# Kernel tuning notes

Hardware: AMD Instinct MI355X
Metric: run time of the kernel (lower is better)

## Reference

```python
import jax, jax.numpy as jnp
import numpy as np

LAMBDA_ENTROPY = 0.1
LAMBDA_REPULSION = 0.5
LAMBDA_INTER = 0.3
TEMPERATURE = 1.0
EPS = 1e-8


def setup_inputs() -> dict:
    key = jax.random.key(0)
    k1, k2 = jax.random.split(key)
    membership = jax.random.uniform(k1, (16384, 64, 32), dtype=jnp.float32)   # (N,F,K) soft bin assignments
    teacher_preds = jax.random.uniform(k2, (16384, 128), dtype=jnp.float32)   # (N,C)
    return {"membership": membership, "teacher_preds": teacher_preds}


def reference(membership, teacher_preds):
    N, F, K = membership.shape
    # --- weighted centroids per (feature, bin) ---
    bin_mass = membership.sum(axis=0) + EPS                       # (F,K)
    sum_weighted_y = jnp.einsum('nfk,nc->fkc', membership, teacher_preds)  # avoids (N,F,K,C)
    centroids = sum_weighted_y / bin_mass[..., None]              # (F,K,C)
    # --- weighted intra-bin variance: ||y_n - c_fk||^2 expanded, no (N,F,K,C) tensor ---
    y_sq = jnp.sum(teacher_preds * teacher_preds, axis=-1)        # (N,)
    c_sq = jnp.sum(centroids * centroids, axis=-1)                # (F,K)
    cross = jnp.einsum('nc,fkc->nfk', teacher_preds, centroids)   # (N,F,K)
    dist_sq = y_sq[:, None, None] + c_sq[None, :, :] - 2.0 * cross
    weighted_variance = jnp.sum(membership * dist_sq, axis=0) / bin_mass  # (F,K)
    loss_dispersion = weighted_variance.sum()
    # --- bin-occupancy entropy ---
    p_bins = bin_mass / N                                         # (F,K)
    loss_entropy = jnp.sum(p_bins * jnp.log(p_bins + EPS))
    # --- neighbor repulsion between adjacent bin centroids ---
    neighbor_dist = jnp.sum((centroids[:, :-1, :] - centroids[:, 1:, :]) ** 2, axis=-1)  # (F,K-1)
    loss_repulsion = jnp.sum(jnp.exp(-neighbor_dist / TEMPERATURE))
    # --- all-pairs inter-bin dispersion, batched over F (replaces python loop) ---
    dots = jnp.einsum('fkc,fjc->fkj', centroids, centroids)       # (F,K,K)
    pairwise = c_sq[:, :, None] + c_sq[:, None, :] - 2.0 * dots
    triu = jnp.triu(jnp.ones((K, K), dtype=centroids.dtype), k=1)  # strictly upper
    loss_inter = jnp.sum(jnp.exp(-pairwise / TEMPERATURE) * triu) / F
    total = (loss_dispersion
             + LAMBDA_ENTROPY * loss_entropy
             + LAMBDA_REPULSION * loss_repulsion
             + LAMBDA_INTER * loss_inter)
    return total, loss_dispersion, loss_entropy, loss_repulsion, loss_inter
```

## Files before the change

### kernel.cpp

```cpp
#include <hip/hip_runtime.h>
#include <math.h>

#define N_PTS   16384
#define F_DIM   64
#define K_BINS  32
#define C_DIM   128
#define FK      2048
#define NB32    (N_PTS / 32)
#define CW      132
#define EPS_F   1e-8f
#define NCHUNK  16
#define CN      1024

typedef _Float16 f16x8 __attribute__((ext_vector_type(8)));
typedef float    f32x4 __attribute__((ext_vector_type(4)));

__global__ __launch_bounds__(256) void build_ybf_k(const float* __restrict__ Y,
                                                   _Float16* __restrict__ Ybf,
                                                   float* __restrict__ accs) {
    __shared__ __align__(16) float Yl[64][132];
    __shared__ float ysql[64];
    const int t  = threadIdx.x;
    if (blockIdx.x == 0 && t < 8) accs[t] = 0.0f;
    const int n0 = blockIdx.x * 64;
    const int nl = t >> 5;
    const int c4 = t & 31;
#pragma unroll
    for (int p = 0; p < 8; ++p) {
        const int n = p * 8 + nl;
        const float4 v = reinterpret_cast<const float4*>(Y + (size_t)(n0 + n) * C_DIM)[c4];
        reinterpret_cast<float4*>(Yl[n])[c4] = v;
        float sq = v.x * v.x + v.y * v.y + v.z * v.z + v.w * v.w;
#pragma unroll
        for (int m = 16; m >= 1; m >>= 1) sq += __shfl_xor(sq, m, 64);
        if (c4 == 0) ysql[n] = sq;
    }
    __syncthreads();
    for (int p = 0; p < 5; ++p) {
        const int s = t + p * 256;
        if (s < 1152) {
            const int nb2  = s / 576;
            const int r    = s % 576;
            const int ct   = r >> 6;
            const int l    = r & 63;
            const int quad = l >> 4, cl = l & 15;
            const int nloc = nb2 * 32 + quad * 8;
            f16x8 v;
            if (ct < 8) {
                const int c = ct * 16 + cl;
#pragma unroll
                for (int j = 0; j < 8; ++j) v[j] = (_Float16)Yl[nloc + j][c];
            } else if (cl == 0) {
#pragma unroll
                for (int j = 0; j < 8; ++j) v[j] = (_Float16)ysql[nloc + j];
            } else if (cl == 1) {
#pragma unroll
                for (int j = 0; j < 8; ++j) v[j] = (_Float16)1.0f;
            } else {
#pragma unroll
                for (int j = 0; j < 8; ++j) v[j] = (_Float16)0.0f;
            }
            const int nb = blockIdx.x * 2 + nb2;
            *reinterpret_cast<f16x8*>(Ybf + ((size_t)(ct * NB32 + nb) * 64 + l) * 8) = v;
        }
    }
}

__global__ __launch_bounds__(256) void gemm_k(const float* __restrict__ M,
                                              const _Float16* __restrict__ Ybf,
                                              float* __restrict__ wpart) {
    __shared__ __align__(16) _Float16 Bb[2][2][9][512];
    const int t    = threadIdx.x;
    const int fk0  = blockIdx.x * 32;
    const int ch   = blockIdx.y;
    const int w    = t >> 6;
    const int g    = w >> 1;
    const int wl   = w & 1;
    const int l    = t & 63;
    const int quad = l >> 4;
    const int cl   = l & 15;
    const int fkA  = fk0 + wl * 16 + cl;
    const float* mp = M + fkA;
    const int n0   = ch * CN + g * 512;
    const int nb0  = n0 >> 5;

    f32x4 acc[9] = {};
    float ar[3][8];

#define WAITVM(n) asm volatile("s_waitcnt vmcnt(" #n ")" ::: "memory")
#define STAGE(s, par)                                                          \
    {                                                                          \
        const int nb_ = nb0 + (s);                                             \
        _Pragma("unroll")                                                      \
        for (int ct = wl; ct < 9; ct += 2) {                                   \
            const _Float16* g_ = Ybf + ((size_t)(ct * NB32 + nb_) * 64 + l) * 8; \
            __builtin_amdgcn_global_load_lds(                                  \
                (const __attribute__((address_space(1))) unsigned*)g_,         \
                (__attribute__((address_space(3))) unsigned*)&Bb[g][par][ct][0], \
                16, 0, 0);                                                     \
        }                                                                      \
    }
#define LOADA(s)                                                               \
    {                                                                          \
        const size_t nbase_ = (size_t)(n0 + (s) * 32 + quad * 8);              \
        _Pragma("unroll")                                                      \
        for (int j = 0; j < 8; ++j) ar[(s) % 3][j] = mp[(nbase_ + j) * FK];    \
    }
#define SBAR0() __builtin_amdgcn_sched_barrier(0)

    STAGE(0, 0); SBAR0(); LOADA(0); SBAR0();
    STAGE(1, 1); SBAR0(); LOADA(1); SBAR0(); LOADA(2); SBAR0();

#pragma unroll
    for (int s = 0; s < 16; ++s) {
        if (s < 14)       WAITVM(20);
        else if (s == 14) WAITVM(12);
        else              WAITVM(0);
        __builtin_amdgcn_s_barrier();
        SBAR0();
        f16x8 bf[9];
#pragma unroll
        for (int ct = 0; ct < 9; ++ct)
            bf[ct] = *reinterpret_cast<const f16x8*>(&Bb[g][s & 1][ct][l * 8]);
        f16x8 af;
#pragma unroll
        for (int j = 0; j < 8; ++j) af[j] = (_Float16)ar[s % 3][j];
        asm volatile("s_waitcnt lgkmcnt(0)" ::: "memory");
        SBAR0();
        __builtin_amdgcn_s_barrier();
        SBAR0();
        if (s + 2 < 16) STAGE(s + 2, s & 1);
        SBAR0();
        if (s + 3 < 16) LOADA(s + 3);
        SBAR0();
        __builtin_amdgcn_s_setprio(1);
#pragma unroll
        for (int ct = 0; ct < 9; ++ct)
            acc[ct] = __builtin_amdgcn_mfma_f32_16x16x32_f16(af, bf[ct], acc[ct], 0, 0, 0);
        __builtin_amdgcn_s_setprio(0);
    }
#undef WAITVM
#undef STAGE
#undef LOADA
#undef SBAR0

    __syncthreads();
    float* scr = reinterpret_cast<float*>(&Bb[0][0][0][0]);
    if (g == 1) {
#pragma unroll
        for (int ct = 0; ct < 9; ++ct)
#pragma unroll
            for (int r = 0; r < 4; ++r)
                scr[(wl * 16 + quad * 4 + r) * 144 + ct * 16 + cl] = acc[ct][r];
    }
    __syncthreads();
    if (g == 0) {
        float* wp = wpart + (size_t)ch * FK * CW;
#pragma unroll
        for (int ct = 0; ct < 9; ++ct) {
            const int c = ct * 16 + cl;
            if (c < CW) {
#pragma unroll
                for (int r = 0; r < 4; ++r) {
                    const int row = wl * 16 + quad * 4 + r;
                    const int fk  = fk0 + row;
                    wp[(size_t)fk * CW + c] = acc[ct][r] + scr[row * 144 + c];
                }
            }
        }
    }
}

__global__ __launch_bounds__(128) void reduce_w_k(const float* __restrict__ wpart,
                                                  float* __restrict__ W, int nchunk) {
    const int idx = blockIdx.x * 128 + threadIdx.x;
    const float4* src = reinterpret_cast<const float4*>(wpart);
    const size_t cs = (size_t)FK * CW / 4;
    float4 s0 = make_float4(0.f, 0.f, 0.f, 0.f), s1 = s0, s2 = s0, s3 = s0;
    int ch = 0;
    for (; ch + 3 < nchunk; ch += 4) {
        const float4 a = src[idx + (size_t)(ch + 0) * cs];
        const float4 b = src[idx + (size_t)(ch + 1) * cs];
        const float4 c = src[idx + (size_t)(ch + 2) * cs];
        const float4 d = src[idx + (size_t)(ch + 3) * cs];
        s0.x += a.x; s0.y += a.y; s0.z += a.z; s0.w += a.w;
        s1.x += b.x; s1.y += b.y; s1.z += b.z; s1.w += b.w;
        s2.x += c.x; s2.y += c.y; s2.z += c.z; s2.w += c.w;
        s3.x += d.x; s3.y += d.y; s3.z += d.z; s3.w += d.w;
    }
    for (; ch < nchunk; ++ch) {
        const float4 a = src[idx + (size_t)ch * cs];
        s0.x += a.x; s0.y += a.y; s0.z += a.z; s0.w += a.w;
    }
    float4 r;
    r.x = (s0.x + s1.x) + (s2.x + s3.x);
    r.y = (s0.y + s1.y) + (s2.y + s3.y);
    r.z = (s0.z + s1.z) + (s2.z + s3.z);
    r.w = (s0.w + s1.w) + (s2.w + s3.w);
    reinterpret_cast<float4*>(W)[idx] = r;
}

__global__ __launch_bounds__(256) void epilogue_k(const float* __restrict__ W,
                                                  float* __restrict__ accs,
                                                  float* __restrict__ out) {
    __shared__ __align__(16) float Wl[32][CW];
    __shared__ float Bv[32], Binv[32], S1v[32], csq[32];
    __shared__ float scr[32][8];
    __shared__ float4 red4[256];
    const int t = threadIdx.x;
    const int f = blockIdx.x;

    for (int e = t; e < 32 * 33; e += 256) {
        const int k = e / 33, c4 = e % 33;
        reinterpret_cast<float4*>(Wl[k])[c4] =
            reinterpret_cast<const float4*>(W + (size_t)(f * 32 + k) * CW)[c4];
    }
    __syncthreads();
    if (t < 32) {
        const float B = Wl[t][129] + EPS_F;
        Bv[t] = B; Binv[t] = 1.0f / B; S1v[t] = Wl[t][128];
    }
    __syncthreads();
    {
        const int k = t >> 3, g = t & 7;
        const float ib = Binv[k];
        float s = 0.f;
        for (int c = g * 16; c < g * 16 + 16; ++c) {
            const float v = Wl[k][c] * ib;
            Wl[k][c] = v;
            s = fmaf(v, v, s);
        }
        scr[k][g] = s;
    }
    __syncthreads();
    if (t < 32) {
        float s = 0.f;
#pragma unroll
        for (int g = 0; g < 8; ++g) s += scr[t][g];
        csq[t] = s;
    }
    __syncthreads();

    float my_disp = 0.f, my_ent = 0.f, my_rep = 0.f, my_inter = 0.f;
    if (t < 32) {
        my_disp = (S1v[t] - csq[t] * (Bv[t] + EPS_F)) * Binv[t];
        const float p = Bv[t] * (1.0f / (float)N_PTS);
        my_ent = p * logf(p + EPS_F);
    }
    {
        const int pr = t >> 3, g = t & 7;
        float s = 0.f;
        if (pr < 31) {
            for (int c = g * 16; c < g * 16 + 16; ++c) {
                const float d = Wl[pr][c] - Wl[pr + 1][c];
                s = fmaf(d, d, s);
            }
        }
        __syncthreads();
        scr[pr][g] = s;
    }
    __syncthreads();
    if (t < 31) {
        float d = 0.f;
#pragma unroll
        for (int g = 0; g < 8; ++g) d += scr[t][g];
        my_rep = expf(-d);
    }
#pragma unroll
    for (int s4 = 0; s4 < 4; ++s4) {
        const int slot = t + s4 * 256;
        const int k = slot >> 5, j = slot & 31;
        if (k < j) {
            float dot = 0.f;
            for (int c4 = 0; c4 < 32; ++c4) {
                const float4 a = reinterpret_cast<const float4*>(Wl[k])[c4];
                const float4 b = reinterpret_cast<const float4*>(Wl[j])[c4];
                dot = fmaf(a.x, b.x, dot); dot = fmaf(a.y, b.y, dot);
                dot = fmaf(a.z, b.z, dot); dot = fmaf(a.w, b.w, dot);
            }
            my_inter += expf(-(csq[k] + csq[j] - 2.0f * dot));
        }
    }
    red4[t] = make_float4(my_disp, my_ent, my_rep, my_inter);
    __syncthreads();
    for (int off = 128; off >= 1; off >>= 1) {
        if (t < off) {
            const float4 a = red4[t], b = red4[t + off];
            red4[t] = make_float4(a.x + b.x, a.y + b.y, a.z + b.z, a.w + b.w);
        }
        __syncthreads();
    }
    if (t == 0) {
        atomicAdd(accs + 0, red4[0].x);
        atomicAdd(accs + 1, red4[0].y);
        atomicAdd(accs + 2, red4[0].z);
        atomicAdd(accs + 3, red4[0].w);
        __threadfence();
        const unsigned prev = __hip_atomic_fetch_add(
            reinterpret_cast<unsigned*>(accs + 4), 1u,
            __ATOMIC_ACQ_REL, __HIP_MEMORY_SCOPE_AGENT);
        if (prev == (unsigned)(F_DIM - 1)) {
            const float disp = __hip_atomic_load(accs + 0, __ATOMIC_RELAXED, __HIP_MEMORY_SCOPE_AGENT);
            const float ent  = __hip_atomic_load(accs + 1, __ATOMIC_RELAXED, __HIP_MEMORY_SCOPE_AGENT);
            const float rep  = __hip_atomic_load(accs + 2, __ATOMIC_RELAXED, __HIP_MEMORY_SCOPE_AGENT);
            const float inter = __hip_atomic_load(accs + 3, __ATOMIC_RELAXED, __HIP_MEMORY_SCOPE_AGENT)
                                * (1.0f / (float)F_DIM);
            out[0] = disp + 0.1f * ent + 0.5f * rep + 0.3f * inter;
            out[1] = disp;
            out[2] = ent;
            out[3] = rep;
            out[4] = inter;
        }
    }
}

extern "C" void kernel_launch(void* const* d_in, const int* in_sizes, int n_in,
                              void* d_out, int out_size, void* d_ws, size_t ws_size,
                              hipStream_t stream) {
    const float* M = (const float*)d_in[0];
    const float* Y = (const float*)d_in[1];
    float* out = (float*)d_out;
    char*  ws  = (char*)d_ws;

    const size_t ybfBytes = (size_t)9 * NB32 * 64 * 8 * sizeof(_Float16);
    const size_t wBytes   = (size_t)FK * CW * sizeof(float);

    _Float16* Ybf   = (_Float16*)ws;
    float*    W     = (float*)(ws + ybfBytes);
    float*    accs  = (float*)(ws + ybfBytes + wBytes);
    float*    wpart = (float*)(ws + ybfBytes + wBytes + 1024);

    build_ybf_k<<<dim3(N_PTS / 64), dim3(256), 0, stream>>>(Y, Ybf, accs);
    gemm_k<<<dim3(64, NCHUNK), dim3(256), 0, stream>>>(M, Ybf, wpart);
    reduce_w_k<<<dim3(FK * CW / 4 / 128), dim3(128), 0, stream>>>(wpart, W, NCHUNK);
    epilogue_k<<<dim3(F_DIM), dim3(256), 0, stream>>>(W, accs, out);
}
```

Before: 234.5 us.

## Replace LDS-staged B pipeline with direct register double-buffered global loads

The GEMM kernel drops the async global-to-LDS staging of the f16 teacher tiles, along with its barriers, vmcnt waits and priority hints. Each wave now loads its nine B fragments straight from global memory into a two-deep register buffer alongside the A loads. This removes the LDS traffic and block-wide synchronisation per step. In exchange, the two waves sharing a group each fetch all nine B tiles instead of splitting them, which doubles B global loads, raises register pressure, and gives a shallower prefetch distance.

```diff
diff --git a/kernel.cpp b/kernel.cpp
--- a/kernel.cpp
+++ b/kernel.cpp
@@ -69,7 +69,7 @@
 __global__ __launch_bounds__(256) void gemm_k(const float* __restrict__ M,
                                               const _Float16* __restrict__ Ybf,
                                               float* __restrict__ wpart) {
-    __shared__ __align__(16) _Float16 Bb[2][2][9][512];
+    __shared__ __align__(16) float scr[32][144];
     const int t    = threadIdx.x;
     const int fk0  = blockIdx.x * 32;
     const int ch   = blockIdx.y;
@@ -79,79 +79,48 @@
     const int l    = t & 63;
     const int quad = l >> 4;
     const int cl   = l & 15;
-    const int fkA  = fk0 + wl * 16 + cl;
-    const float* mp = M + fkA;
+    const float* mp = M + fk0 + wl * 16 + cl;
     const int n0   = ch * CN + g * 512;
     const int nb0  = n0 >> 5;
+    const _Float16* yb = Ybf + ((size_t)nb0 * 64 + l) * 8;
 
     f32x4 acc[9] = {};
-    float ar[3][8];
-
-#define WAITVM(n) asm volatile("s_waitcnt vmcnt(" #n ")" ::: "memory")
-#define STAGE(s, par)                                                          \
-    {                                                                          \
-        const int nb_ = nb0 + (s);                                             \
-        _Pragma("unroll")                                                      \
-        for (int ct = wl; ct < 9; ct += 2) {                                   \
-            const _Float16* g_ = Ybf + ((size_t)(ct * NB32 + nb_) * 64 + l) * 8; \
-            __builtin_amdgcn_global_load_lds(                                  \
-                (const __attribute__((address_space(1))) unsigned*)g_,         \
-                (__attribute__((address_space(3))) unsigned*)&Bb[g][par][ct][0], \
-                16, 0, 0);                                                     \
-        }                                                                      \
-    }
-#define LOADA(s)                                                               \
+    f16x8 bf[2][9];
+    float ar[2][8];
+
+#define LOADB(buf, s)                                                          \
+    _Pragma("unroll")                                                          \
+    for (int ct = 0; ct < 9; ++ct)                                             \
+        bf[buf][ct] = *reinterpret_cast<const f16x8*>(                         \
+            yb + ((size_t)ct * NB32 + (s)) * 64 * 8);
+#define LOADA(buf, s)                                                          \
     {                                                                          \
         const size_t nbase_ = (size_t)(n0 + (s) * 32 + quad * 8);              \
         _Pragma("unroll")                                                      \
-        for (int j = 0; j < 8; ++j) ar[(s) % 3][j] = mp[(nbase_ + j) * FK];    \
-    }
-#define SBAR0() __builtin_amdgcn_sched_barrier(0)
-
-    STAGE(0, 0); SBAR0(); LOADA(0); SBAR0();
-    STAGE(1, 1); SBAR0(); LOADA(1); SBAR0(); LOADA(2); SBAR0();
-
+        for (int j = 0; j < 8; ++j) ar[buf][j] = mp[(nbase_ + j) * FK];        \
+    }
+
+    LOADB(0, 0); LOADA(0, 0);
 #pragma unroll
     for (int s = 0; s < 16; ++s) {
-        if (s < 14)       WAITVM(20);
-        else if (s == 14) WAITVM(12);
-        else              WAITVM(0);
-        __builtin_amdgcn_s_barrier();
-        SBAR0();
-        f16x8 bf[9];
+        const int cur = s & 1, nxt = cur ^ 1;
+        if (s + 1 < 16) { LOADB(nxt, s + 1); LOADA(nxt, s + 1); }
+        f16x8 af;
+#pragma unroll
+        for (int j = 0; j < 8; ++j) af[j] = (_Float16)ar[cur][j];
 #pragma unroll
         for (int ct = 0; ct < 9; ++ct)
-            bf[ct] = *reinterpret_cast<const f16x8*>(&Bb[g][s & 1][ct][l * 8]);
-        f16x8 af;
-#pragma unroll
-        for (int j = 0; j < 8; ++j) af[j] = (_Float16)ar[s % 3][j];
-        asm volatile("s_waitcnt lgkmcnt(0)" ::: "memory");
-        SBAR0();
-        __builtin_amdgcn_s_barrier();
-        SBAR0();
-        if (s + 2 < 16) STAGE(s + 2, s & 1);
-        SBAR0();
-        if (s + 3 < 16) LOADA(s + 3);
-        SBAR0();
-        __builtin_amdgcn_s_setprio(1);
+            acc[ct] = __builtin_amdgcn_mfma_f32_16x16x32_f16(af, bf[cur][ct], acc[ct], 0, 0, 0);
+    }
+#undef LOADB
+#undef LOADA
+
+    if (g == 1) {
 #pragma unroll
         for (int ct = 0; ct < 9; ++ct)
-            acc[ct] = __builtin_amdgcn_mfma_f32_16x16x32_f16(af, bf[ct], acc[ct], 0, 0, 0);
-        __builtin_amdgcn_s_setprio(0);
-    }
-#undef WAITVM
-#undef STAGE
-#undef LOADA
-#undef SBAR0
-
-    __syncthreads();
-    float* scr = reinterpret_cast<float*>(&Bb[0][0][0][0]);
-    if (g == 1) {
-#pragma unroll
-        for (int ct = 0; ct < 9; ++ct)
 #pragma unroll
             for (int r = 0; r < 4; ++r)
-                scr[(wl * 16 + quad * 4 + r) * 144 + ct * 16 + cl] = acc[ct][r];
+                scr[wl * 16 + quad * 4 + r][ct * 16 + cl] = acc[ct][r];
     }
     __syncthreads();
     if (g == 0) {
@@ -164,7 +133,7 @@
                 for (int r = 0; r < 4; ++r) {
                     const int row = wl * 16 + quad * 4 + r;
                     const int fk  = fk0 + row;
-                    wp[(size_t)fk * CW + c] = acc[ct][r] + scr[row * 144 + c];
+                    wp[(size_t)fk * CW + c] = acc[ct][r] + scr[row][c];
                 }
             }
         }
```

Result: slower. 256.3 us (+9.3%).
